# Optimization experiments

Hardware: AMD Instinct MI355X
Metric: run time of the kernel (lower is better)

The kernel has to match this reference:

```python
import jax, jax.numpy as jnp
import numpy as np

NUM_EMBEDDINGS = 8192
EMBEDDING_DIM = 512
COMMITMENT_COST = 0.25


def setup_inputs() -> dict:
    key = jax.random.key(0)
    kx, ke = jax.random.split(key)
    x = jax.random.normal(kx, (32, 512, EMBEDDING_DIM), dtype=jnp.float32)
    # nn.Embedding weight initialized uniform(-1/K, 1/K)
    emb = jax.random.uniform(ke, (NUM_EMBEDDINGS, EMBEDDING_DIM), dtype=jnp.float32,
                             minval=-1.0 / NUM_EMBEDDINGS, maxval=1.0 / NUM_EMBEDDINGS)
    return {"x": x, "emb": emb}


def reference(x, emb):
    sg = jax.lax.stop_gradient
    D = emb.shape[1]
    flat = x.reshape(-1, D)  # [N, D]
    # squared euclidean distances via ||a||^2 + ||b||^2 - 2 a.b  -> [N, K]
    distances = (jnp.sum(flat ** 2, axis=1, keepdims=True)
                 + jnp.sum(emb ** 2, axis=1)
                 - 2.0 * flat @ emb.T)
    encoding_indices = jnp.argmin(distances, axis=1)  # [N]
    quantized = emb[encoding_indices].reshape(x.shape)
    e_latent_loss = jnp.mean((sg(quantized) - x) ** 2)
    q_latent_loss = jnp.mean((quantized - sg(x)) ** 2)
    loss = q_latent_loss + COMMITMENT_COST * e_latent_loss
    quantized_st = x + sg(quantized - x)  # straight-through estimator
    # Faithful to the original (buggy) perplexity: torch.bincount has length
    # max(idx)+1 = L; mean(counts/N) over L bins == 1/L (a scalar).
    L = (jnp.max(encoding_indices) + 1).astype(x.dtype)
    avg_probs = 1.0 / L
    perplexity = jnp.exp(-avg_probs * jnp.log(avg_probs + 1e-10))
    return quantized_st, loss, perplexity, encoding_indices.reshape(-1, 1)
```

## Files before the change

### kernel.cpp

```cpp
#include <hip/hip_runtime.h>
#include <math.h>

#define N_ROWS   16384
#define DIM      512
#define DQV      128
#define K_CODES  8192
#define NSPLIT   2
#define KHALF    (K_CODES / NSPLIT)
#define BM       128
#define BK       512
#define BD       8
#define DCS      (DIM / BD)
#define NSTRIP   (KHALF / BK)
#define THREADS  1024
#define EPI_BM   64

#define OUT_LOSS 8388608
#define OUT_PERP 8388609
#define OUT_IDX  8388610

#define WS_XX    0
#define WS_BV0   65536
#define WS_BI0   131072
#define WS_BV1   196608
#define WS_BI1   262144
#define WS_LOSS  327680
#define WS_MAXI  327688

__global__ void init_ws(double* ws_loss, int* ws_maxidx) {
    *ws_loss = 0.0;
    *ws_maxidx = 0;
}

__device__ __forceinline__ float p128_sq(const float4* p) {
    float4 q0 = p[0], q1 = p[1];
    float r0 = __fmul_rn(q0.x, q0.x), r1 = __fmul_rn(q0.y, q0.y);
    float r2 = __fmul_rn(q0.z, q0.z), r3 = __fmul_rn(q0.w, q0.w);
    float r4 = __fmul_rn(q1.x, q1.x), r5 = __fmul_rn(q1.y, q1.y);
    float r6 = __fmul_rn(q1.z, q1.z), r7 = __fmul_rn(q1.w, q1.w);
    #pragma unroll
    for (int t = 1; t < 16; ++t) {
        q0 = p[2 * t]; q1 = p[2 * t + 1];
        r0 = __fadd_rn(r0, __fmul_rn(q0.x, q0.x));
        r1 = __fadd_rn(r1, __fmul_rn(q0.y, q0.y));
        r2 = __fadd_rn(r2, __fmul_rn(q0.z, q0.z));
        r3 = __fadd_rn(r3, __fmul_rn(q0.w, q0.w));
        r4 = __fadd_rn(r4, __fmul_rn(q1.x, q1.x));
        r5 = __fadd_rn(r5, __fmul_rn(q1.y, q1.y));
        r6 = __fadd_rn(r6, __fmul_rn(q1.z, q1.z));
        r7 = __fadd_rn(r7, __fmul_rn(q1.w, q1.w));
    }
    return __fadd_rn(__fadd_rn(__fadd_rn(r0, r1), __fadd_rn(r2, r3)),
                     __fadd_rn(__fadd_rn(r4, r5), __fadd_rn(r6, r7)));
}

__global__ __launch_bounds__(256) void xx_kernel(const float4* __restrict__ x4,
                                                 float* __restrict__ xx) {
    int row = blockIdx.x * 256 + threadIdx.x;
    const float4* p = x4 + (size_t)row * DQV;
    float a = p128_sq(p);
    float b = p128_sq(p + 32);
    float c = p128_sq(p + 64);
    float d = p128_sq(p + 96);
    xx[row] = __fadd_rn(__fadd_rn(a, b), __fadd_rn(c, d));
}

__global__ __launch_bounds__(256) void xt_kernel(const float* __restrict__ x,
                                                 float* __restrict__ xt) {
    __shared__ float t[64][65];
    const int bn = blockIdx.x;
    const int bd = blockIdx.y;
    const int tx = threadIdx.x & 15;
    const int ty = threadIdx.x >> 4;
    #pragma unroll
    for (int i = 0; i < 4; ++i) {
        int nl = 16 * i + ty;
        float4 v = *(const float4*)(x + (size_t)(bn * 64 + nl) * DIM + bd * 64 + 4 * tx);
        t[4 * tx + 0][nl] = v.x;
        t[4 * tx + 1][nl] = v.y;
        t[4 * tx + 2][nl] = v.z;
        t[4 * tx + 3][nl] = v.w;
    }
    __syncthreads();
    #pragma unroll
    for (int i = 0; i < 4; ++i) {
        int dl = 16 * i + ty;
        float4 w;
        w.x = t[dl][4 * tx + 0];
        w.y = t[dl][4 * tx + 1];
        w.z = t[dl][4 * tx + 2];
        w.w = t[dl][4 * tx + 3];
        *(float4*)(xt + (size_t)(bd * 64 + dl) * N_ROWS + bn * 64 + 4 * tx) = w;
    }
}

__global__ __launch_bounds__(THREADS, 4)
void vq_main(const float* __restrict__ xt,
             const float* __restrict__ emb,
             const float* __restrict__ xx,
             float* __restrict__ bv0,
             int* __restrict__ bi0,
             float* __restrict__ bv1,
             int* __restrict__ bi1) {
    __shared__ float Et[2][BD * BK];

    const int tid  = threadIdx.x;
    const int lane = tid & 63;
    const int wv   = tid >> 6;
    const int wvu  = __builtin_amdgcn_readfirstlane(wv);
    const int rt   = blockIdx.x >> 1;
    const int h    = blockIdx.x & 1;
    const int r0   = rt * BM;
    const int kb   = h * KHALF;
    const int rwu  = r0 + (wvu << 3);

    const float4* emb4 = (const float4*)emb;
    const float4* xt4  = (const float4*)xt;
    const int cc = tid & 511;
    const int dh = tid >> 9;

    float bestv[8];
    int   besti[8];
    #pragma unroll
    for (int i = 0; i < 8; ++i) { bestv[i] = 3.402823466e38f; besti[i] = 0; }

    float4 pe = emb4[(size_t)(kb + cc) * DQV + dh];

    for (int kc = 0; kc < NSTRIP; ++kc) {
        const int k0 = kb + kc * BK;

        float acc[8][8];
        #pragma unroll
        for (int i = 0; i < 8; ++i)
            #pragma unroll
            for (int j = 0; j < 8; ++j) acc[i][j] = 0.0f;

        __syncthreads();
        {
            const int db = 4 * dh;
            Et[0][(db + 0) * BK + cc] = pe.x;
            Et[0][(db + 1) * BK + cc] = pe.y;
            Et[0][(db + 2) * BK + cc] = pe.z;
            Et[0][(db + 3) * BK + cc] = pe.w;
        }

        for (int dc = 0; dc < DCS; ++dc) {
            const int buf = dc & 1;
            __syncthreads();

            {
                int nk0, ndq;
                if (dc < DCS - 1) { nk0 = k0; ndq = 2 * (dc + 1) + dh; }
                else { nk0 = (kc < NSTRIP - 1) ? k0 + BK : kb; ndq = dh; }
                pe = emb4[(size_t)(nk0 + cc) * DQV + ndq];
            }

            const int dbase = dc * BD;
            #pragma unroll
            for (int dd = 0; dd < BD; ++dd) {
                const float4* xp4 = xt4 + (size_t)(dbase + dd) * (N_ROWS / 4) + (rwu >> 2);
                float4 xa = xp4[0], xb = xp4[1];
                const float* ep = &Et[buf][dd * BK + 4 * lane];
                float4 e0 = *(const float4*)(ep);
                float4 e1 = *(const float4*)(ep + 256);
                float xs[8] = {xa.x, xa.y, xa.z, xa.w, xb.x, xb.y, xb.z, xb.w};
                float ev[8] = {e0.x, e0.y, e0.z, e0.w, e1.x, e1.y, e1.z, e1.w};
                #pragma unroll
                for (int i = 0; i < 8; ++i)
                    #pragma unroll
                    for (int j = 0; j < 8; ++j)
                        acc[i][j] = __fmaf_rn(xs[i], ev[j], acc[i][j]);
            }

            if (dc < DCS - 1) {
                const int nb = buf ^ 1;
                const int db = 4 * dh;
                Et[nb][(db + 0) * BK + cc] = pe.x;
                Et[nb][(db + 1) * BK + cc] = pe.y;
                Et[nb][(db + 2) * BK + cc] = pe.z;
                Et[nb][(db + 3) * BK + cc] = pe.w;
            }
        }

        #pragma unroll
        for (int i = 0; i < 8; ++i) {
            float xr_n = xx[rwu + i];
            #pragma unroll
            for (int j2 = 0; j2 < 2; ++j2) {
                #pragma unroll
                for (int t = 0; t < 4; ++t) {
                    float s = __fmaf_rn(-2.0f, acc[i][4 * j2 + t], xr_n);
                    int code = k0 + 256 * j2 + 4 * lane + t;
                    if (s < bestv[i]) { bestv[i] = s; besti[i] = code; }
                }
            }
        }
    }

    #pragma unroll
    for (int i = 0; i < 8; ++i) {
        float v  = bestv[i];
        int  idx = besti[i];
        #pragma unroll
        for (int off = 32; off > 0; off >>= 1) {
            float vv = __shfl_down(v, off);
            int   ii = __shfl_down(idx, off);
            if (vv < v || (vv == v && ii < idx)) { v = vv; idx = ii; }
        }
        if (lane == 0) {
            if (h == 0) { bv0[rwu + i] = v; bi0[rwu + i] = idx; }
            else        { bv1[rwu + i] = v; bi1[rwu + i] = idx; }
        }
    }
}

__global__ __launch_bounds__(256) void vq_epi(const float* __restrict__ x,
                                              const float* __restrict__ emb,
                                              const float* __restrict__ bv0,
                                              const int* __restrict__ bi0,
                                              const float* __restrict__ bv1,
                                              const int* __restrict__ bi1,
                                              float* __restrict__ out,
                                              double* __restrict__ ws_loss,
                                              int* __restrict__ ws_maxidx) {
    __shared__ int idxRow[EPI_BM];
    const int tid = threadIdx.x;
    const int r0  = blockIdx.x * EPI_BM;
    const float4* x4   = (const float4*)x;
    const float4* emb4 = (const float4*)emb;
    float4*       out4 = (float4*)out;

    if (tid < EPI_BM) {
        int row = r0 + tid;
        float v0 = bv0[row]; int i0 = bi0[row];
        float v1 = bv1[row]; int i1 = bi1[row];
        int idx = (v1 < v0) ? i1 : i0;
        idxRow[tid] = idx;
        out[OUT_IDX + row] = (float)idx;
        atomicMax(ws_maxidx, idx);
    }
    __syncthreads();

    double lsum = 0.0;
    for (int i = tid; i < EPI_BM * DQV; i += 256) {
        int row = i >> 7, dq = i & 127;
        int ki  = idxRow[row];
        float4 q  = emb4[(size_t)ki * DQV + dq];
        float4 xv = x4[(size_t)(r0 + row) * DQV + dq];
        float d0 = q.x - xv.x, d1 = q.y - xv.y, d2 = q.z - xv.z, d3 = q.w - xv.w;
        lsum += (double)d0 * (double)d0 + (double)d1 * (double)d1
              + (double)d2 * (double)d2 + (double)d3 * (double)d3;
        float4 o;
        o.x = xv.x + d0; o.y = xv.y + d1; o.z = xv.z + d2; o.w = xv.w + d3;
        out4[(size_t)(r0 + row) * DQV + dq] = o;
    }
    #pragma unroll
    for (int off = 32; off > 0; off >>= 1) lsum += __shfl_down(lsum, off);
    if ((tid & 63) == 0) atomicAdd(ws_loss, lsum);
}

__global__ void vq_final(const double* __restrict__ ws_loss,
                         const int* __restrict__ ws_maxidx,
                         float* __restrict__ out) {
    if (threadIdx.x == 0) {
        double mean = *ws_loss / (double)((size_t)N_ROWS * DIM);
        out[OUT_LOSS] = (float)(1.25 * mean);
        double L   = (double)(*ws_maxidx + 1);
        double avg = 1.0 / L;
        out[OUT_PERP] = (float)exp(-avg * log(avg + 1e-10));
    }
}

extern "C" void kernel_launch(void* const* d_in, const int* in_sizes, int n_in,
                              void* d_out, int out_size, void* d_ws, size_t ws_size,
                              hipStream_t stream) {
    const float* x   = (const float*)d_in[0];
    const float* emb = (const float*)d_in[1];
    float* out = (float*)d_out;

    char* ws = (char*)d_ws;
    float*  xx        = (float*)(ws + WS_XX);
    float*  bv0       = (float*)(ws + WS_BV0);
    int*    bi0       = (int*)  (ws + WS_BI0);
    float*  bv1       = (float*)(ws + WS_BV1);
    int*    bi1       = (int*)  (ws + WS_BI1);
    double* ws_loss   = (double*)(ws + WS_LOSS);
    int*    ws_maxidx = (int*)  (ws + WS_MAXI);

    float* xt = out;

    hipLaunchKernelGGL(init_ws, dim3(1), dim3(1), 0, stream, ws_loss, ws_maxidx);
    hipLaunchKernelGGL(xx_kernel, dim3(N_ROWS / 256), dim3(256), 0, stream,
                       (const float4*)x, xx);
    hipLaunchKernelGGL(xt_kernel, dim3(N_ROWS / 64, DIM / 64), dim3(256), 0, stream,
                       x, xt);
    hipLaunchKernelGGL(vq_main, dim3((N_ROWS / BM) * NSPLIT), dim3(THREADS), 0, stream,
                       xt, emb, xx, bv0, bi0, bv1, bi1);
    hipLaunchKernelGGL(vq_epi, dim3(N_ROWS / EPI_BM), dim3(256), 0, stream,
                       x, emb, bv0, bi0, bv1, bi1, out, ws_loss, ws_maxidx);
    hipLaunchKernelGGL(vq_final, dim3(1), dim3(64), 0, stream,
                       ws_loss, ws_maxidx, out);
}
```

Before: 1.816 ms.

## Stage x tile in shared memory and unroll double-buffer loop by two

The x operand tile (8 dims × 128 rows) is now staged in LDS, double-buffered alongside the embedding tile, where before each wave read it directly from global memory every dd step. The d-chunk loop is manually unrolled by two so the buffer indices are compile-time constants and the prefetch addressing is simpler. This cuts redundant global/L1 traffic for x, whose reads were uniform per wave, in exchange for extra LDS space and LDS reads, and it may change occupancy.

```diff
diff --git a/kernel.cpp b/kernel.cpp
--- a/kernel.cpp
+++ b/kernel.cpp
@@ -94,6 +94,25 @@
     }
 }
 
+__device__ __forceinline__ void fma_tile(const float* __restrict__ etb,
+                                         const float* __restrict__ xtb,
+                                         float acc[8][8]) {
+    #pragma unroll
+    for (int dd = 0; dd < BD; ++dd) {
+        float4 xa = *(const float4*)(xtb + dd * BM);
+        float4 xb = *(const float4*)(xtb + dd * BM + 4);
+        float4 e0 = *(const float4*)(etb + dd * BK);
+        float4 e1 = *(const float4*)(etb + dd * BK + 256);
+        float xs[8] = {xa.x, xa.y, xa.z, xa.w, xb.x, xb.y, xb.z, xb.w};
+        float ev[8] = {e0.x, e0.y, e0.z, e0.w, e1.x, e1.y, e1.z, e1.w};
+        #pragma unroll
+        for (int i = 0; i < 8; ++i)
+            #pragma unroll
+            for (int j = 0; j < 8; ++j)
+                acc[i][j] = __fmaf_rn(xs[i], ev[j], acc[i][j]);
+    }
+}
+
 __global__ __launch_bounds__(THREADS, 4)
 void vq_main(const float* __restrict__ xt,
              const float* __restrict__ emb,
@@ -103,6 +122,7 @@
              float* __restrict__ bv1,
              int* __restrict__ bi1) {
     __shared__ float Et[2][BD * BK];
+    __shared__ float Xt[2][BD * BM];
 
     const int tid  = threadIdx.x;
     const int lane = tid & 63;
@@ -115,9 +135,20 @@
     const int rwu  = r0 + (wvu << 3);
 
     const float4* emb4 = (const float4*)emb;
-    const float4* xt4  = (const float4*)xt;
     const int cc = tid & 511;
     const int dh = tid >> 9;
+    const int xd = tid >> 7;
+    const int xr = tid & 127;
+
+    float* esb0 = &Et[0][(4 * dh) * BK + cc];
+    float* esb1 = &Et[1][(4 * dh) * BK + cc];
+    float* xsb0 = &Xt[0][xd * BM + xr];
+    float* xsb1 = &Xt[1][xd * BM + xr];
+    const float* etb0 = &Et[0][4 * lane];
+    const float* etb1 = &Et[1][4 * lane];
+    const float* xtb0 = &Xt[0][wvu << 3];
+    const float* xtb1 = &Xt[1][wvu << 3];
+    const float* pxb = xt + (size_t)xd * N_ROWS + r0 + xr;
 
     float bestv[8];
     int   besti[8];
@@ -125,6 +156,7 @@
     for (int i = 0; i < 8; ++i) { bestv[i] = 3.402823466e38f; besti[i] = 0; }
 
     float4 pe = emb4[(size_t)(kb + cc) * DQV + dh];
+    float  px = pxb[0];
 
     for (int kc = 0; kc < NSTRIP; ++kc) {
         const int k0 = kb + kc * BK;
@@ -136,49 +168,30 @@
             for (int j = 0; j < 8; ++j) acc[i][j] = 0.0f;
 
         __syncthreads();
-        {
-            const int db = 4 * dh;
-            Et[0][(db + 0) * BK + cc] = pe.x;
-            Et[0][(db + 1) * BK + cc] = pe.y;
-            Et[0][(db + 2) * BK + cc] = pe.z;
-            Et[0][(db + 3) * BK + cc] = pe.w;
-        }
-
-        for (int dc = 0; dc < DCS; ++dc) {
-            const int buf = dc & 1;
+        esb0[0] = pe.x; esb0[BK] = pe.y; esb0[2 * BK] = pe.z; esb0[3 * BK] = pe.w;
+        xsb0[0] = px;
+
+        for (int dc = 0; dc < DCS; dc += 2) {
             __syncthreads();
-
-            {
-                int nk0, ndq;
-                if (dc < DCS - 1) { nk0 = k0; ndq = 2 * (dc + 1) + dh; }
-                else { nk0 = (kc < NSTRIP - 1) ? k0 + BK : kb; ndq = dh; }
-                pe = emb4[(size_t)(nk0 + cc) * DQV + ndq];
+            pe = emb4[(size_t)(k0 + cc) * DQV + (2 * (dc + 1) + dh)];
+            px = pxb[(size_t)(dc + 1) * BD * N_ROWS];
+            fma_tile(etb0, xtb0, acc);
+            esb1[0] = pe.x; esb1[BK] = pe.y; esb1[2 * BK] = pe.z; esb1[3 * BK] = pe.w;
+            xsb1[0] = px;
+
+            __syncthreads();
+            if (dc + 2 < DCS) {
+                pe = emb4[(size_t)(k0 + cc) * DQV + (2 * (dc + 2) + dh)];
+                px = pxb[(size_t)(dc + 2) * BD * N_ROWS];
+            } else {
+                const int nk0 = (kc < NSTRIP - 1) ? k0 + BK : kb;
+                pe = emb4[(size_t)(nk0 + cc) * DQV + dh];
+                px = pxb[0];
             }
-
-            const int dbase = dc * BD;
-            #pragma unroll
-            for (int dd = 0; dd < BD; ++dd) {
-                const float4* xp4 = xt4 + (size_t)(dbase + dd) * (N_ROWS / 4) + (rwu >> 2);
-                float4 xa = xp4[0], xb = xp4[1];
-                const float* ep = &Et[buf][dd * BK + 4 * lane];
-                float4 e0 = *(const float4*)(ep);
-                float4 e1 = *(const float4*)(ep + 256);
-                float xs[8] = {xa.x, xa.y, xa.z, xa.w, xb.x, xb.y, xb.z, xb.w};
-                float ev[8] = {e0.x, e0.y, e0.z, e0.w, e1.x, e1.y, e1.z, e1.w};
-                #pragma unroll
-                for (int i = 0; i < 8; ++i)
-                    #pragma unroll
-                    for (int j = 0; j < 8; ++j)
-                        acc[i][j] = __fmaf_rn(xs[i], ev[j], acc[i][j]);
-            }
-
-            if (dc < DCS - 1) {
-                const int nb = buf ^ 1;
-                const int db = 4 * dh;
-                Et[nb][(db + 0) * BK + cc] = pe.x;
-                Et[nb][(db + 1) * BK + cc] = pe.y;
-                Et[nb][(db + 2) * BK + cc] = pe.z;
-                Et[nb][(db + 3) * BK + cc] = pe.w;
+            fma_tile(etb1, xtb1, acc);
+            if (dc + 2 < DCS) {
+                esb0[0] = pe.x; esb0[BK] = pe.y; esb0[2 * BK] = pe.z; esb0[3 * BK] = pe.w;
+                xsb0[0] = px;
             }
         }
 
```

New measurement: 2.144 ms. 1.18x slower.
